# Performance work log

Hardware: AMD Instinct MI355X
Metric: run time of the kernel (lower is better)

Reference implementation:

```python
import jax, jax.numpy as jnp
import numpy as np

WIDTH = 256
HEAD = 16
SCALE = 2
G = WIDTH // HEAD          # 16 groups
NH = G * SCALE             # 32 kernelized heads
EPS = 1e-5
N_NODES = 20000
B_GRAPHS = 1024


def setup_inputs() -> dict:
    key = jax.random.key(0)
    ks = jax.random.split(key, 10)
    x = jax.random.normal(ks[0], (N_NODES, WIDTH), jnp.float32)
    x_res = jax.random.normal(ks[1], (B_GRAPHS, NH, HEAD, HEAD), jnp.float32)
    batch = jnp.sort(jax.random.randint(ks[2], (N_NODES,), 0, B_GRAPHS)).astype(jnp.int64)
    w_pre = jax.random.normal(ks[3], (WIDTH, WIDTH), jnp.float32) * 0.02
    b_pre = jnp.zeros((WIDTH,), jnp.float32)
    # grouped 1x1 convs: [groups, width_scale, head_out, head_in]
    wq = jax.random.normal(ks[4], (G, SCALE, HEAD, HEAD), jnp.float32) * 0.02
    wk = jax.random.normal(ks[5], (G, SCALE, HEAD, HEAD), jnp.float32) * 0.02
    wv = jax.random.normal(ks[6], (G, SCALE, HEAD, HEAD), jnp.float32) * 0.02
    w_post = jax.random.normal(ks[7], (WIDTH, WIDTH * SCALE), jnp.float32) * 0.02
    b_post = jnp.zeros((WIDTH,), jnp.float32)
    log_scale = jnp.full((WIDTH,), np.log(0.01), jnp.float32)
    return {"x": x, "x_res": x_res, "batch": batch, "batch_size": B_GRAPHS,
            "w_pre": w_pre, "b_pre": b_pre, "wq": wq, "wk": wk, "wv": wv,
            "w_post": w_post, "b_post": b_post, "log_scale": log_scale}


def reference(x, x_res, batch, batch_size, w_pre, b_pre, wq, wk, wv, w_post, b_post, log_scale):
    n = x.shape[0]
    # pre: 1x1 conv (= linear) + GroupNorm(affine=False); L=1 so normalize over
    # each group's width_head channels.
    y = x @ w_pre.T + b_pre                       # [N, width]
    yg = y.reshape(n, G, HEAD)                    # [N, G, Hd]
    mu = yg.mean(-1, keepdims=True)
    var = yg.var(-1, keepdims=True)               # biased, as in GroupNorm
    yn = (yg - mu) / jnp.sqrt(var + EPS)          # [N, G, Hd]

    inv_sqrt_h = 1.0 / np.sqrt(HEAD)
    # grouped convs -> kernelized q,k (exp) and v
    xq = jnp.exp(jnp.einsum('ngi,gsoi->ngso', yn, wq) * inv_sqrt_h).reshape(n, NH, HEAD)
    xk = jnp.exp(jnp.einsum('ngi,gsoi->ngso', yn, wk) * inv_sqrt_h).reshape(n, NH, HEAD)
    xv = jnp.einsum('ngi,gsoi->ngso', yn, wv).reshape(n, NH, HEAD)

    # outer product k (x) v then scatter-sum over graphs  [B, NH, Hd, Hd]
    kv = jnp.einsum('bnh,bnv->bnhv', xk, xv)
    kv_sum = jax.ops.segment_sum(kv, batch, num_segments=batch_size) + x_res
    x_res_out = kv_sum

    # per-graph key sum, gathered back to nodes
    k_sum = jax.ops.segment_sum(xk, batch, num_segments=batch_size)[batch]  # [N, NH, Hd]
    denom = jnp.einsum('bnh,bnh->bn', xq, k_sum)                            # [N, NH]
    qn = xq / denom[:, :, None]

    out = jnp.einsum('bnh,bnhv->bnv', qn, kv_sum[batch]).reshape(n, WIDTH * SCALE)
    out = jnp.exp(log_scale) * (out @ w_post.T + b_post)                    # [N, width]
    return (out, x_res_out)
```

## Files before the change

### kernel.cpp

```cpp
#include <hip/hip_runtime.h>
#include <stdint.h>

typedef unsigned int u32;
typedef unsigned short u16;
typedef __attribute__((ext_vector_type(8))) short v8s;
typedef __attribute__((ext_vector_type(4))) float v4f;

#define GN_EPS 1e-5f

__device__ __forceinline__ float bflo(u32 u){ return __uint_as_float(u << 16); }
__device__ __forceinline__ float bfhi(u32 u){ return __uint_as_float(u & 0xffff0000u); }
__device__ __forceinline__ float bf1(u16 u){ return __uint_as_float((u32)u << 16); }
__device__ __forceinline__ u16 f2bf(float f){
  u32 x = __float_as_uint(f);
  u32 r = (x + 0x7fffu + ((x >> 16) & 1u)) >> 16;
  return (u16)r;
}
__device__ __forceinline__ u32 pack2(float a, float b){
  return (u32)f2bf(a) | ((u32)f2bf(b) << 16);
}
__device__ __forceinline__ void unpack8(const uint4 u, float* f){
  f[0]=bflo(u.x); f[1]=bfhi(u.x); f[2]=bflo(u.y); f[3]=bfhi(u.y);
  f[4]=bflo(u.z); f[5]=bfhi(u.z); f[6]=bflo(u.w); f[7]=bfhi(u.w);
}
__device__ __forceinline__ uint4 loadpack8(const float* __restrict__ p){
  float4 a = *(const float4*)p, b = *(const float4*)(p + 4);
  return make_uint4(pack2(a.x,a.y),pack2(a.z,a.w),pack2(b.x,b.y),pack2(b.z,b.w));
}
__device__ __forceinline__ float dot16(const float* __restrict__ yn,
                                       const float* __restrict__ row){
  float4 W0 = *(const float4*)row;
  float4 W1 = *(const float4*)(row + 4);
  float4 W2 = *(const float4*)(row + 8);
  float4 W3 = *(const float4*)(row + 12);
  float d = 0.f;
  d = fmaf(yn[0],W0.x,d); d = fmaf(yn[1],W0.y,d);
  d = fmaf(yn[2],W0.z,d); d = fmaf(yn[3],W0.w,d);
  d = fmaf(yn[4],W1.x,d); d = fmaf(yn[5],W1.y,d);
  d = fmaf(yn[6],W1.z,d); d = fmaf(yn[7],W1.w,d);
  d = fmaf(yn[8],W2.x,d); d = fmaf(yn[9],W2.y,d);
  d = fmaf(yn[10],W2.z,d); d = fmaf(yn[11],W2.w,d);
  d = fmaf(yn[12],W3.x,d); d = fmaf(yn[13],W3.y,d);
  d = fmaf(yn[14],W3.z,d); d = fmaf(yn[15],W3.w,d);
  return d;
}
__device__ __forceinline__ float rsum16(float v){
  v += __shfl_xor(v, 1);
  v += __shfl_xor(v, 2);
  v += __shfl_xor(v, 4);
  v += __shfl_xor(v, 8);
  return v;
}

__device__ __forceinline__ int getb(const int* __restrict__ b, int is64, int i){
  return b[is64 ? 2*i : i];
}

__global__ __launch_bounds__(256) void k_detect(
    const int* __restrict__ batch, int n, int* __restrict__ flags)
{
  int i = blockIdx.x*256 + threadIdx.x;
  int bad = 0;
  if (i < n - 1 && batch[i] > batch[i + 1]) bad = 1;
  if (__builtin_amdgcn_ballot_w64(bad) != 0 && (threadIdx.x & 63) == 0)
    atomicOr(&flags[0], 1);
}

__global__ __launch_bounds__(256) void k_bounds(
    const int* __restrict__ batch, const int* __restrict__ flags,
    int N, int B, int* __restrict__ bounds)
{
  int i = blockIdx.x*256 + threadIdx.x;
  if (i >= N) return;
  const int is64 = flags[0];
  int b = getb(batch, is64, i);
  int prev = (i == 0) ? -1 : getb(batch, is64, i - 1);
  for (int g = prev + 1; g <= b; g++) bounds[g] = i;
  if (i == N - 1)
    for (int g = b + 1; g <= B; g++) bounds[g] = N;
}

__global__ __launch_bounds__(256) void k_prefused(
    const float* __restrict__ x, const float* __restrict__ wpre,
    const float* __restrict__ bpre,
    const float* __restrict__ wq, const float* __restrict__ wk,
    const float* __restrict__ wv,
    u16* __restrict__ qo, u16* __restrict__ ko, u16* __restrict__ vo,
    int N, int nbm)
{
  __shared__ __align__(16) char SMEM[25600];
  __shared__ __align__(16) u16 ynL[128*74];
  u16* As = (u16*)SMEM;
  u16* Bs = (u16*)(SMEM + 128*40*2);
  float* wL = (float*)SMEM;

  const int t = threadIdx.x;
  const int bm = blockIdx.x % nbm;
  const int bn = blockIdx.x / nbm;
  const int m_base = bm*128, n_base = bn*64;
  const int w = t >> 6, lane = t & 63;
  const int wr = (w >> 1)*64, wc = (w & 1)*32;
  const int fr = lane & 15, fk = lane >> 4;
  const int arow = t >> 1, acol = (t & 1)*16;
  const int brow = t >> 2, bcol = (t & 3)*8;

  v4f acc[4][2];
#pragma unroll
  for (int i = 0; i < 4; i++)
#pragma unroll
    for (int j = 0; j < 2; j++) acc[i][j] = (v4f){0.f,0.f,0.f,0.f};

  for (int k0 = 0; k0 < 256; k0 += 32) {
    __syncthreads();
    {
      int gm = m_base + arow;
      uint4 a0 = make_uint4(0u,0u,0u,0u), a1 = make_uint4(0u,0u,0u,0u);
      if (gm < N) {
        a0 = loadpack8(x + (size_t)gm*256 + k0 + acol);
        a1 = loadpack8(x + (size_t)gm*256 + k0 + acol + 8);
      }
      *(uint4*)&As[arow*40 + acol]     = a0;
      *(uint4*)&As[arow*40 + acol + 8] = a1;
      uint4 bv = loadpack8(wpre + (size_t)(n_base + brow)*256 + k0 + bcol);
      *(uint4*)&Bs[brow*40 + bcol] = bv;
    }
    __syncthreads();
    v8s b0 = *(const v8s*)&Bs[(wc      + fr)*40 + fk*8];
    v8s b1 = *(const v8s*)&Bs[(wc + 16 + fr)*40 + fk*8];
#pragma unroll
    for (int mi = 0; mi < 4; mi++) {
      v8s a = *(const v8s*)&As[(wr + mi*16 + fr)*40 + fk*8];
      acc[mi][0] = __builtin_amdgcn_mfma_f32_16x16x32_bf16(a,b0,acc[mi][0],0,0,0);
      acc[mi][1] = __builtin_amdgcn_mfma_f32_16x16x32_bf16(a,b1,acc[mi][1],0,0,0);
    }
  }

#pragma unroll
  for (int nj = 0; nj < 2; nj++) {
    int col = n_base + wc + nj*16 + fr;
    float bpv = bpre[col];
    int gloc = (w & 1)*2 + nj;
#pragma unroll
    for (int mi = 0; mi < 4; mi++) {
#pragma unroll
      for (int r = 0; r < 4; r++) {
        float yv = acc[mi][nj][r] + bpv;
        float s1 = rsum16(yv);
        float s2 = rsum16(yv*yv);
        float mu = s1 * 0.0625f;
        float var = fmaxf(s2*0.0625f - mu*mu, 0.f);
        float ynv = (yv - mu) * rsqrtf(var + GN_EPS);
        int row = wr + mi*16 + fk*4 + r;
        ynL[row*74 + gloc*16 + fr] = f2bf(ynv);
      }
    }
  }
  __syncthreads();

  {
    const float* srcs[3] = {wq, wk, wv};
#pragma unroll
    for (int tz = 0; tz < 3; tz++) {
      for (int i = t; i < 2048; i += 256) {
        int gi = i >> 9, rem = i & 511;
        wL[tz*2080 + gi*520 + rem] = srcs[tz][((size_t)(bn*4 + gi))*512 + rem];
      }
    }
  }
  __syncthreads();

  u16* outs[3] = {qo, ko, vo};
  const int gl = w;
  const int g  = bn*4 + gl;
#pragma unroll
  for (int p = 0; p < 2; p++) {
    int nloc = p*64 + lane;
    int node = m_base + nloc;
    if (node >= N) continue;
    u32 yw[8];
#pragma unroll
    for (int j = 0; j < 8; j++)
      yw[j] = *(const u32*)&ynL[nloc*74 + gl*16 + j*2];
    float yn[16];
#pragma unroll
    for (int j = 0; j < 8; j++) { yn[2*j] = bflo(yw[j]); yn[2*j+1] = bfhi(yw[j]); }
#pragma unroll
    for (int tz = 0; tz < 3; tz++) {
#pragma unroll
      for (int s = 0; s < 2; s++) {
        u32 pk[8];
#pragma unroll
        for (int o = 0; o < 16; o++) {
          float d = dot16(yn, &wL[tz*2080 + gl*520 + (s*16 + o)*16]);
          if (tz < 2) d = __expf(d*0.25f);
          if (o & 1) pk[o>>1] |= (u32)f2bf(d) << 16;
          else       pk[o>>1]  = (u32)f2bf(d);
        }
        u16* dst = outs[tz] + (size_t)node*512 + g*32 + s*16;
        *(uint4*)dst       = make_uint4(pk[0],pk[1],pk[2],pk[3]);
        *(uint4*)(dst + 8) = make_uint4(pk[4],pk[5],pk[6],pk[7]);
      }
    }
  }
}

__global__ __launch_bounds__(512) void k_segatt(
    const u16* __restrict__ xk, const u16* __restrict__ xv,
    const u16* __restrict__ xq, const float* __restrict__ xres,
    const int* __restrict__ bounds,
    float* __restrict__ out1, u16* __restrict__ att, int N)
{
  __shared__ __align__(16) u16 kvs[32*280];
  __shared__ float kss[32*17];
  const int b = blockIdx.x, t = threadIdx.x;
  const int lo = bounds[b], hi = bounds[b+1];
  const int nh = t >> 4, d = t & 15;

  float kv[16];
#pragma unroll
  for (int v = 0; v < 16; v++) kv[v] = 0.f;
  float ks = 0.f;

  const size_t koff = (size_t)nh*16 + d;
  const size_t voff = (size_t)nh*16;
  int node = lo;
  for (; node + 1 < hi; node += 2) {
    u16  ka  = xk[(size_t)node*512 + koff];
    uint4 Va0 = *(const uint4*)(xv + (size_t)node*512 + voff);
    uint4 Va1 = *(const uint4*)(xv + (size_t)node*512 + voff + 8);
    u16  kb  = xk[(size_t)(node+1)*512 + koff];
    uint4 Vb0 = *(const uint4*)(xv + (size_t)(node+1)*512 + voff);
    uint4 Vb1 = *(const uint4*)(xv + (size_t)(node+1)*512 + voff + 8);
    float k0 = bf1(ka), k1 = bf1(kb);
    float va[16], vb[16];
    unpack8(Va0, va); unpack8(Va1, va + 8);
    unpack8(Vb0, vb); unpack8(Vb1, vb + 8);
    ks += k0 + k1;
#pragma unroll
    for (int v = 0; v < 16; v++) {
      kv[v] = fmaf(k0, va[v], kv[v]);
      kv[v] = fmaf(k1, vb[v], kv[v]);
    }
  }
  if (node < hi) {
    u16  ka  = xk[(size_t)node*512 + koff];
    uint4 V0 = *(const uint4*)(xv + (size_t)node*512 + voff);
    uint4 V1 = *(const uint4*)(xv + (size_t)node*512 + voff + 8);
    float k0 = bf1(ka);
    float vf[16]; unpack8(V0, vf); unpack8(V1, vf + 8);
    ks += k0;
#pragma unroll
    for (int v = 0; v < 16; v++) kv[v] = fmaf(k0, vf[v], kv[v]);
  }

  kss[nh*17 + d] = ks;

  {
    size_t idx = ((size_t)(b*32 + nh)*16 + d)*16;
    const float* xp = xres + idx;
    float4 X0 = *(const float4*)xp;
    float4 X1 = *(const float4*)(xp + 4);
    float4 X2 = *(const float4*)(xp + 8);
    float4 X3 = *(const float4*)(xp + 12);
    float xf[16] = {X0.x,X0.y,X0.z,X0.w,X1.x,X1.y,X1.z,X1.w,
                    X2.x,X2.y,X2.z,X2.w,X3.x,X3.y,X3.z,X3.w};
    float o[16];
#pragma unroll
    for (int j = 0; j < 16; j++) o[j] = kv[j] + xf[j];
    float* op = out1 + idx;
    *(float4*)op        = make_float4(o[0],o[1],o[2],o[3]);
    *(float4*)(op + 4)  = make_float4(o[4],o[5],o[6],o[7]);
    *(float4*)(op + 8)  = make_float4(o[8],o[9],o[10],o[11]);
    *(float4*)(op + 12) = make_float4(o[12],o[13],o[14],o[15]);
    u16* lp = &kvs[nh*280 + d*16];
    *(uint4*)lp       = make_uint4(pack2(o[0],o[1]),  pack2(o[2],o[3]),
                                   pack2(o[4],o[5]),  pack2(o[6],o[7]));
    *(uint4*)(lp + 8) = make_uint4(pack2(o[8],o[9]),  pack2(o[10],o[11]),
                                   pack2(o[12],o[13]),pack2(o[14],o[15]));
  }
  __syncthreads();

  const int nh2 = t & 31, ns = t >> 5;
  for (int n0 = lo; n0 < hi; n0 += 16) {
    int nodei = n0 + ns;
    if (nodei >= hi) continue;
    const u16* qp = xq + (size_t)nodei*512 + nh2*16;
    uint4 Q0 = *(const uint4*)qp;
    uint4 Q1 = *(const uint4*)(qp + 8);
    float q[16]; unpack8(Q0, q); unpack8(Q1, q + 8);
    const float* ksp = &kss[nh2*17];
    float denom = 0.f;
#pragma unroll
    for (int i = 0; i < 16; i++) denom = fmaf(q[i], ksp[i], denom);
    float inv = 1.0f / fmaxf(denom, 1e-20f);
    float a[16];
#pragma unroll
    for (int v = 0; v < 16; v++) a[v] = 0.f;
    const u16* kvp = &kvs[nh2*280];
#pragma unroll
    for (int h = 0; h < 16; h++) {
      float qh = q[h] * inv;
      uint4 W0 = *(const uint4*)(kvp + h*16);
      uint4 W1 = *(const uint4*)(kvp + h*16 + 8);
      float wv2[16]; unpack8(W0, wv2); unpack8(W1, wv2 + 8);
#pragma unroll
      for (int v = 0; v < 16; v++) a[v] = fmaf(qh, wv2[v], a[v]);
    }
    u32 p[8];
#pragma unroll
    for (int j = 0; j < 8; j++) p[j] = pack2(a[2*j], a[2*j+1]);
    u16* dst = att + (size_t)nodei*512 + nh2*16;
    *(uint4*)dst       = make_uint4(p[0],p[1],p[2],p[3]);
    *(uint4*)(dst + 8) = make_uint4(p[4],p[5],p[6],p[7]);
  }
}

__global__ __launch_bounds__(256) void k_post(
    const u16* __restrict__ att, const float* __restrict__ wpost,
    const float* __restrict__ bpost, const float* __restrict__ ls,
    float* __restrict__ out0, int N, int nbm)
{
  __shared__ __align__(16) u16 As[128*40];
  __shared__ __align__(16) u16 Bs[64*40];
  const int t = threadIdx.x;
  const int bm = blockIdx.x % nbm;
  const int bn = blockIdx.x / nbm;
  const int m_base = bm*128, n_base = bn*64;
  const int w = t >> 6, lane = t & 63;
  const int wr = (w >> 1)*64, wc = (w & 1)*32;
  const int fr = lane & 15, fk = lane >> 4;
  const int arow = t >> 1, acol = (t & 1)*16;
  const int brow = t >> 2, bcol = (t & 3)*8;

  v4f acc[4][2];
#pragma unroll
  for (int i = 0; i < 4; i++)
#pragma unroll
    for (int j = 0; j < 2; j++) acc[i][j] = (v4f){0.f,0.f,0.f,0.f};

  for (int k0 = 0; k0 < 512; k0 += 32) {
    __syncthreads();
    {
      int gm = m_base + arow;
      uint4 a0 = make_uint4(0u,0u,0u,0u), a1 = make_uint4(0u,0u,0u,0u);
      if (gm < N) {
        a0 = *(const uint4*)(att + (size_t)gm*512 + k0 + acol);
        a1 = *(const uint4*)(att + (size_t)gm*512 + k0 + acol + 8);
      }
      *(uint4*)&As[arow*40 + acol]     = a0;
      *(uint4*)&As[arow*40 + acol + 8] = a1;
      uint4 bv = loadpack8(wpost + (size_t)(n_base + brow)*512 + k0 + bcol);
      *(uint4*)&Bs[brow*40 + bcol] = bv;
    }
    __syncthreads();
    v8s b0 = *(const v8s*)&Bs[(wc      + fr)*40 + fk*8];
    v8s b1 = *(const v8s*)&Bs[(wc + 16 + fr)*40 + fk*8];
#pragma unroll
    for (int mi = 0; mi < 4; mi++) {
      v8s a = *(const v8s*)&As[(wr + mi*16 + fr)*40 + fk*8];
      acc[mi][0] = __builtin_amdgcn_mfma_f32_16x16x32_bf16(a,b0,acc[mi][0],0,0,0);
      acc[mi][1] = __builtin_amdgcn_mfma_f32_16x16x32_bf16(a,b1,acc[mi][1],0,0,0);
    }
  }
#pragma unroll
  for (int nj = 0; nj < 2; nj++) {
    int col = n_base + wc + nj*16 + fr;
    float bpv = bpost[col];
    float e   = __expf(ls[col]);
#pragma unroll
    for (int mi = 0; mi < 4; mi++) {
#pragma unroll
      for (int r = 0; r < 4; r++) {
        int row = m_base + wr + mi*16 + fk*4 + r;
        if (row < N) out0[(size_t)row*256 + col] = e*(acc[mi][nj][r] + bpv);
      }
    }
  }
}

extern "C" void kernel_launch(void* const* d_in, const int* in_sizes, int n_in,
                              void* d_out, int out_size, void* d_ws, size_t ws_size,
                              hipStream_t stream)
{
  const float* x     = (const float*)d_in[0];
  const float* xres  = (const float*)d_in[1];
  const int*   batch = (const int*)d_in[2];
  const float* wpre  = (const float*)d_in[4];
  const float* bpre  = (const float*)d_in[5];
  const float* wq    = (const float*)d_in[6];
  const float* wk    = (const float*)d_in[7];
  const float* wv    = (const float*)d_in[8];
  const float* wpost = (const float*)d_in[9];
  const float* bpost = (const float*)d_in[10];
  const float* ls    = (const float*)d_in[11];

  const int N = in_sizes[0] / 256;
  const int B = in_sizes[1] / 8192;
  const int nbm = (N + 127) / 128;
  const int nchunk = (N + 255) / 256;

  char* ws = (char*)d_ws;
  size_t off = 0;
  int*   flags  = (int*)(ws + off); off += 256;
  int*   bounds = (int*)(ws + off); off += ((size_t)B + 64) * 4;
  u16*   att    = (u16*)(ws + off);  off += (size_t)N * 1024;
  u16*   q      = (u16*)(ws + off);  off += (size_t)N * 1024;
  u16*   kten   = (u16*)(ws + off);  off += (size_t)N * 1024;
  u16*   vten   = (u16*)(ws + off);  off += (size_t)N * 1024;

  float* out0 = (float*)d_out;
  float* out1 = out0 + (size_t)N * 256;

  hipMemsetAsync(flags, 0, 4, stream);
  k_detect  <<<nchunk,        256, 0, stream>>>(batch, N, flags);
  k_bounds  <<<nchunk,        256, 0, stream>>>(batch, flags, N, B, bounds);
  k_prefused<<<nbm * 4,       256, 0, stream>>>(x, wpre, bpre, wq, wk, wv,
                                                q, kten, vten, N, nbm);
  k_segatt  <<<B,             512, 0, stream>>>(kten, vten, q, xres, bounds,
                                                out1, att, N);
  k_post    <<<nbm * 4,       256, 0, stream>>>(att, wpost, bpost, ls, out0, N, nbm);
}
```

Before: 128.2 us.

## Widen post GEMM tile to 128 columns; read grouped conv weights from global

The post-projection GEMM tile grows from 128x64 to 128x128, so each wave holds a 4x4 MFMA accumulator block and half as many blocks are launched. This halves how often the attention activation tile is re-read and raises MFMA work per LDS fragment load, at the cost of more registers per thread. Separately, the prefused kernel no longer stages the q/k/v grouped-conv weights in shared memory. It reads them straight from global memory (expected to hit in cache), which drops a staging pass and a barrier but puts scalar global loads inside the inner dot products.

```diff
diff --git a/kernel.cpp b/kernel.cpp
--- a/kernel.cpp
+++ b/kernel.cpp
@@ -88,11 +88,9 @@
     u16* __restrict__ qo, u16* __restrict__ ko, u16* __restrict__ vo,
     int N, int nbm)
 {
-  __shared__ __align__(16) char SMEM[25600];
+  __shared__ __align__(16) u16 As[128*40];
+  __shared__ __align__(16) u16 Bs[64*40];
   __shared__ __align__(16) u16 ynL[128*74];
-  u16* As = (u16*)SMEM;
-  u16* Bs = (u16*)(SMEM + 128*40*2);
-  float* wL = (float*)SMEM;
 
   const int t = threadIdx.x;
   const int bm = blockIdx.x % nbm;
@@ -157,19 +155,8 @@
   }
   __syncthreads();
 
-  {
-    const float* srcs[3] = {wq, wk, wv};
-#pragma unroll
-    for (int tz = 0; tz < 3; tz++) {
-      for (int i = t; i < 2048; i += 256) {
-        int gi = i >> 9, rem = i & 511;
-        wL[tz*2080 + gi*520 + rem] = srcs[tz][((size_t)(bn*4 + gi))*512 + rem];
-      }
-    }
-  }
-  __syncthreads();
-
   u16* outs[3] = {qo, ko, vo};
+  const float* wsrc[3] = {wq, wk, wv};
   const int gl = w;
   const int g  = bn*4 + gl;
 #pragma unroll
@@ -186,12 +173,13 @@
     for (int j = 0; j < 8; j++) { yn[2*j] = bflo(yw[j]); yn[2*j+1] = bfhi(yw[j]); }
 #pragma unroll
     for (int tz = 0; tz < 3; tz++) {
+      const float* wg = wsrc[tz] + (size_t)g*512;
 #pragma unroll
       for (int s = 0; s < 2; s++) {
         u32 pk[8];
 #pragma unroll
         for (int o = 0; o < 16; o++) {
-          float d = dot16(yn, &wL[tz*2080 + gl*520 + (s*16 + o)*16]);
+          float d = dot16(yn, wg + (s*16 + o)*16);
           if (tz < 2) d = __expf(d*0.25f);
           if (o & 1) pk[o>>1] |= (u32)f2bf(d) << 16;
           else       pk[o>>1]  = (u32)f2bf(d);
@@ -321,22 +309,21 @@
     float* __restrict__ out0, int N, int nbm)
 {
   __shared__ __align__(16) u16 As[128*40];
-  __shared__ __align__(16) u16 Bs[64*40];
+  __shared__ __align__(16) u16 Bs[128*40];
   const int t = threadIdx.x;
   const int bm = blockIdx.x % nbm;
   const int bn = blockIdx.x / nbm;
-  const int m_base = bm*128, n_base = bn*64;
+  const int m_base = bm*128, n_base = bn*128;
   const int w = t >> 6, lane = t & 63;
-  const int wr = (w >> 1)*64, wc = (w & 1)*32;
+  const int wr = (w >> 1)*64, wc = (w & 1)*64;
   const int fr = lane & 15, fk = lane >> 4;
   const int arow = t >> 1, acol = (t & 1)*16;
-  const int brow = t >> 2, bcol = (t & 3)*8;
-
-  v4f acc[4][2];
+
+  v4f acc[4][4];
 #pragma unroll
   for (int i = 0; i < 4; i++)
 #pragma unroll
-    for (int j = 0; j < 2; j++) acc[i][j] = (v4f){0.f,0.f,0.f,0.f};
+    for (int j = 0; j < 4; j++) acc[i][j] = (v4f){0.f,0.f,0.f,0.f};
 
   for (int k0 = 0; k0 < 512; k0 += 32) {
     __syncthreads();
@@ -349,21 +336,26 @@
       }
       *(uint4*)&As[arow*40 + acol]     = a0;
       *(uint4*)&As[arow*40 + acol + 8] = a1;
-      uint4 bv = loadpack8(wpost + (size_t)(n_base + brow)*512 + k0 + bcol);
-      *(uint4*)&Bs[brow*40 + bcol] = bv;
+      uint4 b0 = loadpack8(wpost + (size_t)(n_base + arow)*512 + k0 + acol);
+      uint4 b1 = loadpack8(wpost + (size_t)(n_base + arow)*512 + k0 + acol + 8);
+      *(uint4*)&Bs[arow*40 + acol]     = b0;
+      *(uint4*)&Bs[arow*40 + acol + 8] = b1;
     }
     __syncthreads();
-    v8s b0 = *(const v8s*)&Bs[(wc      + fr)*40 + fk*8];
-    v8s b1 = *(const v8s*)&Bs[(wc + 16 + fr)*40 + fk*8];
+    v8s bfr[4];
+#pragma unroll
+    for (int j = 0; j < 4; j++)
+      bfr[j] = *(const v8s*)&Bs[(wc + j*16 + fr)*40 + fk*8];
 #pragma unroll
     for (int mi = 0; mi < 4; mi++) {
       v8s a = *(const v8s*)&As[(wr + mi*16 + fr)*40 + fk*8];
-      acc[mi][0] = __builtin_amdgcn_mfma_f32_16x16x32_bf16(a,b0,acc[mi][0],0,0,0);
-      acc[mi][1] = __builtin_amdgcn_mfma_f32_16x16x32_bf16(a,b1,acc[mi][1],0,0,0);
-    }
-  }
-#pragma unroll
-  for (int nj = 0; nj < 2; nj++) {
+#pragma unroll
+      for (int j = 0; j < 4; j++)
+        acc[mi][j] = __builtin_amdgcn_mfma_f32_16x16x32_bf16(a,bfr[j],acc[mi][j],0,0,0);
+    }
+  }
+#pragma unroll
+  for (int nj = 0; nj < 4; nj++) {
     int col = n_base + wc + nj*16 + fr;
     float bpv = bpost[col];
     float e   = __expf(ls[col]);
@@ -418,5 +410,5 @@
                                                 q, kten, vten, N, nbm);
   k_segatt  <<<B,             512, 0, stream>>>(kten, vten, q, xres, bounds,
                                                 out1, att, N);
-  k_post    <<<nbm * 4,       256, 0, stream>>>(att, wpost, bpost, ls, out0, N, nbm);
-}
+  k_post    <<<nbm * 2,       256, 0, stream>>>(att, wpost, bpost, ls, out0, N, nbm);
+}
```

Measured after the change: 178.0 us. +38.9%, slower.
